# Kernel optimization log

Hardware: AMD Instinct MI355X
Metric: run time of the kernel (lower is better)

## Reference

```python
import jax, jax.numpy as jnp
import numpy as np


def _layernorm(x, g, b, eps=1e-6):
    mu = jnp.mean(x, -1, keepdims=True)
    var = jnp.var(x, -1, keepdims=True)
    return (x - mu) * jax.lax.rsqrt(var + eps) * g + b


def _rope_interleave(x, cos, sin):
    # de-interleave pairs (x0,x1),(x2,x3),... -> [evens | odds]  (matches
    # torch view(..., d//2, 2).transpose(-1,-2).reshape(..., d))
    x = jnp.concatenate([x[..., 0::2], x[..., 1::2]], axis=-1)
    d = x.shape[-1]
    x1, x2 = x[..., : d // 2], x[..., d // 2 :]
    rot = jnp.concatenate([-x2, x1], axis=-1)
    return x * cos + rot * sin


def setup_inputs() -> dict:
    key = jax.random.key(0)
    k = jax.random.split(key, 6)
    T, H, D, R, HID, QLR, K = 2048, 32, 128, 64, 4096, 1536, 256
    hidden_states = jax.random.normal(k[0], (1, T, HID), jnp.float32)
    q_latent = jax.random.normal(k[1], (1, T, QLR), jnp.float32)
    wq_b = jax.random.normal(k[2], (QLR, H * D), jnp.float32) * 0.02
    wk = jax.random.normal(k[3], (HID, D), jnp.float32) * 0.02
    w_proj = jax.random.normal(k[4], (HID, H), jnp.float32) * 0.02
    k_gamma = jnp.ones((D,), jnp.float32)
    k_beta = jnp.zeros((D,), jnp.float32)
    # real rotary cos/sin tables for the 64-dim rope slice
    pos = jnp.arange(T, dtype=jnp.float32)
    inv_freq = 1.0 / (10000.0 ** (jnp.arange(0, R, 2, dtype=jnp.float32) / R))
    freqs = jnp.outer(pos, inv_freq)
    emb = jnp.concatenate([freqs, freqs], axis=-1)  # [T, R]
    cos, sin = jnp.cos(emb), jnp.sin(emb)
    ks = jnp.zeros((T,), jnp.int32)
    ke = jnp.arange(1, T + 1, dtype=jnp.int32)  # causal: keys [0, t]
    return dict(hidden_states=hidden_states, q_latent=q_latent, ks=ks, ke=ke,
                cos=cos, sin=sin, wq_b=wq_b, wk=wk, k_gamma=k_gamma,
                k_beta=k_beta, w_proj=w_proj, index_topk=K)


def reference(hidden_states, q_latent, ks, ke, cos, sin, wq_b, wk,
              k_gamma, k_beta, w_proj, index_topk):
    T = hidden_states.shape[1]
    H = w_proj.shape[1]
    D = wk.shape[1]
    R = cos.shape[-1]
    weight_scale = (D ** -0.5) * (H ** -0.5)

    q = (q_latent[0] @ wq_b).reshape(T, H, D)              # [T,H,D]
    k = _layernorm(hidden_states[0] @ wk, k_gamma, k_beta)  # [T,D]
    w = hidden_states[0] @ w_proj                           # [T,H]

    q_pe = _rope_interleave(q[..., :R], cos[:, None, :], sin[:, None, :])
    k_pe = _rope_interleave(k[..., :R], cos, sin)
    q = jnp.concatenate([q_pe, q[..., R:]], axis=-1)
    k = jnp.concatenate([k_pe, k[..., R:]], axis=-1)

    # lightning-indexer score: I[t,s] = sum_h w[t,h] * relu(q[t,h] . k[s])
    scores = jnp.einsum('thd,sd->ths', q, k)                # [T,H,S]
    scores = jnp.einsum('ths,th->ts', jax.nn.relu(scores), w) * weight_scale

    j = jnp.arange(T)
    mask = (j[None, :] >= ks[:, None]) & (j[None, :] < ke[:, None])
    scores = jnp.where(mask, scores, -1e30)
    values, idx = jax.lax.top_k(scores, index_topk)
    return idx.reshape(1, T, 1, index_topk), values
```

## Files before the change

kernel.cpp:

```cpp
#include <hip/hip_runtime.h>
#include <cstdint>

typedef unsigned short u16;
typedef unsigned int   u32;
typedef unsigned long long u64;

typedef short bf16x8 __attribute__((ext_vector_type(8)));
typedef float f32x4  __attribute__((ext_vector_type(4)));
typedef u16   u16x8  __attribute__((ext_vector_type(8)));

__device__ __forceinline__ u16 f2b(float f){
  u32 u = __float_as_uint(f);
  u += 0x7FFFu + ((u >> 16) & 1u);
  return (u16)(u >> 16);
}
__device__ __forceinline__ float b2f(u16 h){ return __uint_as_float(((u32)h) << 16); }
__device__ __forceinline__ u32 fkey(float f){
  u32 u = __float_as_uint(f);
  return u ^ ((u & 0x80000000u) ? 0xFFFFFFFFu : 0x80000000u);
}
__device__ __forceinline__ float unkey(u32 k){
  u32 u = (k & 0x80000000u) ? (k ^ 0x80000000u) : ~k;
  return __uint_as_float(u);
}
__device__ __forceinline__ void gload16(const void* g, void* l){
  __builtin_amdgcn_global_load_lds(
      reinterpret_cast<const __attribute__((address_space(1))) char*>(reinterpret_cast<uintptr_t>(g)),
      reinterpret_cast<__attribute__((address_space(3))) char*>(reinterpret_cast<uintptr_t>(l)),
      16, 0, 0);
}

__global__ __launch_bounds__(256) void k_cvt(const float* __restrict__ in, u16* __restrict__ out, int n8){
  int i = blockIdx.x * 256 + threadIdx.x;
  if (i >= n8) return;
  const float4* p = (const float4*)in + (size_t)i * 2;
  float4 a = p[0], b = p[1];
  u16x8 v;
  v[0]=f2b(a.x); v[1]=f2b(a.y); v[2]=f2b(a.z); v[3]=f2b(a.w);
  v[4]=f2b(b.x); v[5]=f2b(b.y); v[6]=f2b(b.z); v[7]=f2b(b.w);
  *((u16x8*)out + i) = v;
}

__global__ __launch_bounds__(256) void k_tcvt(const float* __restrict__ in, u16* __restrict__ out, int R, int C){
  __shared__ float tile[32][33];
  int c0 = blockIdx.x * 32, r0 = blockIdx.y * 32;
  int tx = threadIdx.x & 31, ty = threadIdx.x >> 5;
  for (int i = 0; i < 4; i++){
    int r = ty * 4 + i;
    tile[r][tx] = in[(size_t)(r0 + r) * C + c0 + tx];
  }
  __syncthreads();
  for (int i = 0; i < 4; i++){
    int c = ty * 4 + i;
    out[(size_t)(c0 + c) * R + r0 + tx] = f2b(tile[tx][c]);
  }
}

__global__ __launch_bounds__(256) void k_wct(const float* __restrict__ wk, const float* __restrict__ wp, u16* __restrict__ out){
  __shared__ float tile[32][33];
  int c0 = blockIdx.x * 32, i0 = blockIdx.y * 32;
  int tx = threadIdx.x & 31, ty = threadIdx.x >> 5;
  for (int j = 0; j < 4; j++){
    int i = i0 + ty * 4 + j;
    int c = c0 + tx;
    float v = 0.f;
    if (c < 128) v = wk[(size_t)i * 128 + c];
    else if (c < 160) v = wp[(size_t)i * 32 + (c - 128)];
    tile[ty * 4 + j][tx] = v;
  }
  __syncthreads();
  for (int j = 0; j < 4; j++){
    int c = c0 + ty * 4 + j;
    out[(size_t)c * 4096 + i0 + tx] = f2b(tile[tx][ty * 4 + j]);
  }
}

__global__ __launch_bounds__(256) void k_gemm_kw(const float* __restrict__ A, const u16* __restrict__ B, float* __restrict__ Cp){
  const int Kd = 4096, NC = 192;
  __shared__ float As[128 * 64];
  __shared__ u16 Bs[64 * 64];
  int lin = blockIdx.x;
  int xcd = lin & 7, idx = lin >> 3;
  int nb = idx % 3, pz = idx / 3;
  int p = xcd + 8 * pz;
  int m0 = (p & 15) * 128;
  int kt0 = (p >> 4) * 512;
  int n0 = nb * 64;
  float* C = Cp + (size_t)(p >> 4) * 2048 * NC;
  int tid = threadIdx.x, lane = tid & 63, wid = tid >> 6;
  int wm = wid * 32;
  f32x4 acc[2][4] = {};
  for (int kt = kt0; kt < kt0 + 512; kt += 64){
    for (int c = tid; c < 2048; c += 256){
      int row = c >> 4, off = (c & 15) * 4;
      gload16(A + (size_t)(m0 + row) * Kd + kt + off, (float*)As + (size_t)c * 4);
    }
    for (int c = tid; c < 512; c += 256){
      int row = c >> 3, off = (c & 7) * 8;
      gload16(B + (size_t)(n0 + row) * Kd + kt + off, (u16*)Bs + (size_t)c * 8);
    }
    __syncthreads();
    for (int kk = 0; kk < 2; kk++){
      bf16x8 af[2], bfr[4];
      for (int i = 0; i < 2; i++){
        const float* src = &As[(wm + i * 16 + (lane & 15)) * 64 + kk * 32 + (lane >> 4) * 8];
        f32x4 lo = *(const f32x4*)&src[0];
        f32x4 hi = *(const f32x4*)&src[4];
        bf16x8 t;
        t[0]=(short)f2b(lo[0]); t[1]=(short)f2b(lo[1]); t[2]=(short)f2b(lo[2]); t[3]=(short)f2b(lo[3]);
        t[4]=(short)f2b(hi[0]); t[5]=(short)f2b(hi[1]); t[6]=(short)f2b(hi[2]); t[7]=(short)f2b(hi[3]);
        af[i] = t;
      }
      for (int j = 0; j < 4; j++)
        bfr[j] = *(const bf16x8*)&Bs[(j * 16 + (lane & 15)) * 64 + kk * 32 + (lane >> 4) * 8];
      for (int i = 0; i < 2; i++)
        for (int j = 0; j < 4; j++)
          acc[i][j] = __builtin_amdgcn_mfma_f32_16x16x32_bf16(af[i], bfr[j], acc[i][j], 0, 0, 0);
    }
    __syncthreads();
  }
  for (int i = 0; i < 2; i++)
    for (int j = 0; j < 4; j++){
      int row = m0 + wm + i * 16 + ((lane >> 4) * 4);
      int col = n0 + j * 16 + (lane & 15);
      for (int r = 0; r < 4; r++)
        C[(size_t)(row + r) * NC + col] = acc[i][j][r];
    }
}

__global__ __launch_bounds__(256) void k_lnrope(const float* __restrict__ kwp, const float* __restrict__ gamma,
                                                const float* __restrict__ beta, const float* __restrict__ cosp,
                                                const float* __restrict__ sinp, u16* __restrict__ krot,
                                                float* __restrict__ wfin){
  const size_t ZS = (size_t)2048 * 192;
  int row = blockIdx.x * 4 + (threadIdx.x >> 6);
  int lane = threadIdx.x & 63;
  const float* x = kwp + (size_t)row * 192;
  float2 v = {0.f, 0.f};
  for (int z = 0; z < 8; z++){
    float2 p = *(const float2*)&x[z * ZS + lane * 2];
    v.x += p.x; v.y += p.y;
  }
  float s = v.x + v.y, ss = v.x * v.x + v.y * v.y;
  for (int o = 32; o; o >>= 1){ s += __shfl_xor(s, o); ss += __shfl_xor(ss, o); }
  float mu = s * (1.f / 128.f);
  float var = ss * (1.f / 128.f) - mu * mu;
  float rs = rsqrtf(var + 1e-6f);
  float y0 = (v.x - mu) * rs * gamma[lane * 2]     + beta[lane * 2];
  float y1 = (v.y - mu) * rs * gamma[lane * 2 + 1] + beta[lane * 2 + 1];
  u16* out = krot + (size_t)row * 128;
  if (lane < 32){
    float c = cosp[(size_t)row * 64 + lane], sn = sinp[(size_t)row * 64 + lane];
    out[lane]      = f2b(y0 * c - y1 * sn);
    out[lane + 32] = f2b(y1 * c + y0 * sn);
    float wsum = 0.f;
    for (int z = 0; z < 8; z++) wsum += x[z * ZS + 128 + lane];
    wfin[(size_t)row * 32 + lane] = wsum;
  } else {
    out[lane * 2]     = f2b(y0);
    out[lane * 2 + 1] = f2b(y1);
  }
}

__global__ __launch_bounds__(256) void k_gemm_q(const u16* __restrict__ A, const u16* __restrict__ B,
                                                const float* __restrict__ cosp, const float* __restrict__ sinp,
                                                u16* __restrict__ C){
  const int N = 4096, Kd = 1536;
  __shared__ u16 As[128 * 64];
  __shared__ u16 Bs[128 * 64];
  int linb = blockIdx.x;
  int xcd = linb & 7, loc = linb >> 3;
  int n0 = (xcd * 4 + (loc >> 4)) * 128;
  int m0 = (loc & 15) * 128;
  int tid = threadIdx.x, lane = tid & 63, wid = tid >> 6;
  int wm = (wid >> 1) * 64, wn = (wid & 1) * 64;
  f32x4 acc[4][4] = {};
  for (int kt = 0; kt < Kd; kt += 64){
    for (int c = tid; c < 1024; c += 256){
      int row = c >> 3, off = (c & 7) * 8;
      gload16(A + (size_t)(m0 + row) * Kd + kt + off, (u16*)As + (size_t)c * 8);
      gload16(B + (size_t)(n0 + row) * Kd + kt + off, (u16*)Bs + (size_t)c * 8);
    }
    __syncthreads();
    for (int kk = 0; kk < 2; kk++){
      bf16x8 af[4], bfr[4];
      for (int i = 0; i < 4; i++){
        af[i]  = *(const bf16x8*)&As[(wm + i * 16 + (lane & 15)) * 64 + kk * 32 + (lane >> 4) * 8];
        bfr[i] = *(const bf16x8*)&Bs[(wn + i * 16 + (lane & 15)) * 64 + kk * 32 + (lane >> 4) * 8];
      }
      for (int i = 0; i < 4; i++)
        for (int j = 0; j < 4; j++)
          acc[i][j] = __builtin_amdgcn_mfma_f32_16x16x32_bf16(af[i], bfr[j], acc[i][j], 0, 0, 0);
    }
    __syncthreads();
  }
  if (wn == 0){
    int l = lane & 15;
    int base = lane & 48;
    int sl = base + ((2 * l) & 15);
    for (int i = 0; i < 4; i++){
      int rowb = m0 + wm + i * 16 + ((lane >> 4) * 4);
      f32x4 ne[4];
      for (int j = 0; j < 4; j++){
        int jj = j & 1;
        for (int r = 0; r < 4; r++){
          float eA = __shfl(acc[i][2 * jj][r],     sl);
          float eB = __shfl(acc[i][2 * jj + 1][r], sl);
          float oA = __shfl(acc[i][2 * jj][r],     sl + 1);
          float oB = __shfl(acc[i][2 * jj + 1][r], sl + 1);
          float e = (l >= 8) ? eB : eA;
          float o = (l >= 8) ? oB : oA;
          int row = rowb + r;
          int d = j * 16 + l;
          float c = cosp[(size_t)row * 64 + d];
          float s = sinp[(size_t)row * 64 + d];
          ne[j][r] = (j < 2) ? (e * c - o * s) : (o * c + e * s);
        }
      }
      for (int j = 0; j < 4; j++) acc[i][j] = ne[j];
    }
  }
  for (int i = 0; i < 4; i++)
    for (int j = 0; j < 4; j++){
      int row = m0 + wm + i * 16 + ((lane >> 4) * 4);
      int col = n0 + wn + j * 16 + (lane & 15);
      for (int r = 0; r < 4; r++)
        C[(size_t)(row + r) * N + col] = f2b(acc[i][j][r]);
    }
}

__global__ __launch_bounds__(256, 4) void k_scores(const u16* __restrict__ q, const u16* __restrict__ krot,
                                                   const float* __restrict__ wfin, const int* __restrict__ ke,
                                                   float* __restrict__ S0, float* __restrict__ S1){
  __shared__ u16 Bs[128 * 128];
  __shared__ float Ws[16][32];
  int bid = blockIdx.x;
  int xcd = bid & 7, loc = bid >> 3;
  int hgrp = loc & 1, rest = loc >> 1;
  int sb = rest & 15, j0 = rest >> 4;
  int tb = j0 * 8 + xcd;
  int t0 = tb * 32, s0 = sb * 128;
  int tid = threadIdx.x, lane = tid & 63, wid = tid >> 6;
  int wr = wid >> 1, wc = wid & 1;

  int kev = ke[t0 + (lane & 31)];
  int kemax = kev;
  for (int o = 16; o; o >>= 1) kemax = max(kemax, __shfl_xor(kemax, o));
  if (s0 >= kemax) return;

  for (int c = tid; c < 2048; c += 256)
    gload16(krot + (size_t)(s0 + (c >> 4)) * 128 + (c & 15) * 8, (u16*)Bs + (size_t)c * 8);
  for (int i = tid; i < 512; i += 256){
    int h = i >> 5, r = i & 31;
    Ws[h][r] = wfin[(size_t)(t0 + r) * 32 + hgrp * 16 + h];
  }
  __syncthreads();

  bf16x8 bfr[4][4];
  for (int j = 0; j < 4; j++)
    for (int kc = 0; kc < 4; kc++)
      bfr[j][kc] = *(const bf16x8*)&Bs[(wc * 64 + j * 16 + (lane & 15)) * 128 + kc * 32 + (lane >> 4) * 8];

  f32x4 acc[4] = {};
  const u16* qbase = q + ((size_t)t0 + wr * 16 + (lane & 15)) * 4096 + (size_t)hgrp * 16 * 128 + (lane >> 4) * 8;
  int rbase = wr * 16 + ((lane >> 4) * 4);
  for (int h = 0; h < 16; h++){
    bf16x8 af[4];
    for (int kc = 0; kc < 4; kc++)
      af[kc] = *(const bf16x8*)&qbase[h * 128 + kc * 32];
    f32x4 ah[4] = {};
    for (int kc = 0; kc < 4; kc++)
      for (int j = 0; j < 4; j++)
        ah[j] = __builtin_amdgcn_mfma_f32_16x16x32_bf16(af[kc], bfr[j][kc], ah[j], 0, 0, 0);
    for (int r = 0; r < 4; r++){
      float wv = Ws[h][rbase + r];
      for (int j = 0; j < 4; j++)
        acc[j][r] += fmaxf(ah[j][r], 0.f) * wv;
    }
  }
  float* Sp = hgrp ? S1 : S0;
  for (int j = 0; j < 4; j++){
    int col = s0 + wc * 64 + j * 16 + (lane & 15);
    for (int r = 0; r < 4; r++)
      Sp[(size_t)(t0 + rbase + r) * 2048 + col] = acc[j][r];
  }
}

__global__ __launch_bounds__(256) void k_topk(const float* __restrict__ S0, const float* __restrict__ S1,
                                              const int* __restrict__ ktp, const int* __restrict__ ksv,
                                              const int* __restrict__ ke, float* __restrict__ out){
  int t = blockIdx.x;
  int T = gridDim.x;
  const float* r0 = S0 + (size_t)t * 2048;
  const float* r1 = S1 + (size_t)t * 2048;
  __shared__ u32 keys[2048];
  __shared__ u32 hist[256];
  __shared__ u32 ssum[256];
  __shared__ u32 sb, srem;
  __shared__ u32 wtot[8];
  __shared__ int selIdx[256];
  __shared__ u32 baseGt, baseTie;
  __shared__ u64 skey[256];
  int tid = threadIdx.x;
  int K = ktp[0]; if (K > 256) K = 256;
  int ket = ke[t]; if (ket < 0) ket = 0; if (ket > 2048) ket = 2048;
  int kst = ksv[t]; if (kst < 0) kst = 0;
  int limit = (ket + 255) & ~255;
  if (limit < 256) limit = 256;
  if (limit > 2048) limit = 2048;
  const u32 kneg = fkey(-1e30f);
  const float scale = 0.015625f;
  for (int i4 = tid; i4 < (limit >> 2); i4 += 256){
    int base = i4 * 4;
    float4 a = ((const float4*)r0)[i4];
    float4 b = ((const float4*)r1)[i4];
    float v0 = (a.x + b.x) * scale, v1 = (a.y + b.y) * scale;
    float v2 = (a.z + b.z) * scale, v3 = (a.w + b.w) * scale;
    keys[base + 0] = (base + 0 >= kst && base + 0 < ket) ? fkey(v0) : kneg;
    keys[base + 1] = (base + 1 >= kst && base + 1 < ket) ? fkey(v1) : kneg;
    keys[base + 2] = (base + 2 >= kst && base + 2 < ket) ? fkey(v2) : kneg;
    keys[base + 3] = (base + 3 >= kst && base + 3 < ket) ? fkey(v3) : kneg;
  }
  __syncthreads();
  if (limit > K){
    u32 prefix = 0, pmask = 0, rem = (u32)K;
    for (int p = 3; p >= 0; p--){
      int sh = p * 8;
      hist[tid] = 0;
      __syncthreads();
      for (int i = tid; i < limit; i += 256){
        u32 u = keys[i];
        if ((u & pmask) == prefix) atomicAdd(&hist[(u >> sh) & 255], 1u);
      }
      __syncthreads();
      ssum[tid] = hist[tid];
      __syncthreads();
      for (int off = 1; off < 256; off <<= 1){
        u32 add = (tid + off < 256) ? ssum[tid + off] : 0u;
        __syncthreads();
        ssum[tid] += add;
        __syncthreads();
      }
      u32 mine = ssum[tid];
      u32 above = (tid == 255) ? 0u : ssum[tid + 1];
      if (mine >= rem && above < rem){ sb = (u32)tid; srem = rem - above; }
      __syncthreads();
      prefix |= (sb << sh);
      pmask |= (255u << sh);
      rem = srem;
      __syncthreads();
    }
    u32 thr = prefix;
    int G = K - (int)rem;
    if (tid == 0){ baseGt = 0; baseTie = 0; }
    __syncthreads();
    int nch = limit >> 8;
    for (int ch = 0; ch < nch; ch++){
      int i = ch * 256 + tid;
      u32 u = keys[i];
      bool gt = (u > thr), tie = (u == thr);
      u64 bg = __ballot(gt), bt = __ballot(tie);
      int lane = tid & 63, w = tid >> 6;
      if (lane == 0){ wtot[w] = (u32)__popcll(bg); wtot[4 + w] = (u32)__popcll(bt); }
      __syncthreads();
      u32 og = baseGt, ot = baseTie;
      for (int ww = 0; ww < w; ww++){ og += wtot[ww]; ot += wtot[4 + ww]; }
      og += (u32)__popcll(bg & ((1ull << lane) - 1ull));
      ot += (u32)__popcll(bt & ((1ull << lane) - 1ull));
      if (gt) selIdx[og] = i;
      else if (tie && ot < rem) selIdx[G + ot] = i;
      __syncthreads();
      if (tid == 0){
        for (int ww = 0; ww < 4; ww++){ baseGt += wtot[ww]; baseTie += wtot[4 + ww]; }
      }
      __syncthreads();
    }
    if (tid < K){
      int si = selIdx[tid];
      u32 u = keys[si];
      skey[tid] = ((u64)(~u) << 32) | (u32)si;
    } else {
      skey[tid] = ~0ull;
    }
  } else {
    if (tid < K) skey[tid] = ((u64)(~keys[tid]) << 32) | (u32)tid;
    else skey[tid] = ~0ull;
  }
  __syncthreads();
  for (int size = 2; size <= 256; size <<= 1){
    for (int stride = size >> 1; stride > 0; stride >>= 1){
      int p = tid ^ stride;
      if (p > tid){
        bool up = ((tid & size) == 0);
        u64 a = skey[tid], b = skey[p];
        if ((a > b) == up){ skey[tid] = b; skey[p] = a; }
      }
      __syncthreads();
    }
  }
  if (tid < K){
    u64 sk = skey[tid];
    int idx = (int)(u32)(sk & 0xFFFFFFFFu);
    float val = unkey(~(u32)(sk >> 32));
    out[(size_t)t * K + tid] = (float)idx;
    out[(size_t)T * K + (size_t)t * K + tid] = val;
  }
}

extern "C" void kernel_launch(void* const* d_in, const int* in_sizes, int n_in,
                              void* d_out, int out_size, void* d_ws, size_t ws_size,
                              hipStream_t stream){
  const float* hs   = (const float*)d_in[0];
  const float* ql   = (const float*)d_in[1];
  const int*   ks   = (const int*)  d_in[2];
  const int*   ke   = (const int*)  d_in[3];
  const float* cosp = (const float*)d_in[4];
  const float* sinp = (const float*)d_in[5];
  const float* wqb  = (const float*)d_in[6];
  const float* wk   = (const float*)d_in[7];
  const float* kg   = (const float*)d_in[8];
  const float* kb   = (const float*)d_in[9];
  const float* wp   = (const float*)d_in[10];
  const int*   ktp  = (const int*)  d_in[11];

  char* w = (char*)d_ws;
  u16* qlb = (u16*)w;  w += (size_t)2048 * 1536 * 2;
  u16* wqT = (u16*)w;  w += (size_t)4096 * 1536 * 2;
  u16* wct = (u16*)w;  w += (size_t)192 * 4096 * 2;
  u16* qb  = (u16*)w;  w += (size_t)2048 * 4096 * 2;
  float* kwp = (float*)w; w += (size_t)8 * 2048 * 192 * 4;
  float* wfin = (float*)w; w += (size_t)2048 * 32 * 4;
  u16* krt = (u16*)w;  w += (size_t)2048 * 128 * 2;
  float* S0 = (float*)w; w += (size_t)2048 * 2048 * 4;
  float* S1 = (float*)d_ws;

  hipLaunchKernelGGL(k_cvt, dim3(1536), dim3(256), 0, stream, ql, qlb, 393216);
  hipLaunchKernelGGL(k_tcvt, dim3(128, 48), dim3(256), 0, stream, wqb, wqT, 1536, 4096);
  hipLaunchKernelGGL(k_wct, dim3(6, 128), dim3(256), 0, stream, wk, wp, wct);
  hipLaunchKernelGGL(k_gemm_kw, dim3(384), dim3(256), 0, stream, hs, wct, kwp);
  hipLaunchKernelGGL(k_lnrope, dim3(512), dim3(256), 0, stream, kwp, kg, kb, cosp, sinp, krt, wfin);
  hipLaunchKernelGGL(k_gemm_q, dim3(512), dim3(256), 0, stream, qlb, wqT, cosp, sinp, qb);
  hipLaunchKernelGGL(k_scores, dim3(2048), dim3(256), 0, stream, qb, krt, wfin, ke, S0, S1);
  hipLaunchKernelGGL(k_topk, dim3(2048), dim3(256), 0, stream, S0, S1, ktp, ks, ke, (float*)d_out);
}
```

Measured before the change: 163.0 us.

## Drop head-group split in scores kernel; tile over key blocks instead

The scores kernel previously split the 32 heads into two groups and wrote two partial score matrices that top-k summed. Each block now covers all 32 heads for a 64-key tile, which halves the score write and read traffic and removes the partial-sum add in top-k. Key tiles are narrower, giving finer causal early exit, but each block does twice as many head iterations with half the MFMA columns and reuses each q load over fewer keys.

```diff
diff --git a/kernel.cpp b/kernel.cpp
--- a/kernel.cpp
+++ b/kernel.cpp
@@ -231,15 +231,14 @@
 
 __global__ __launch_bounds__(256, 4) void k_scores(const u16* __restrict__ q, const u16* __restrict__ krot,
                                                    const float* __restrict__ wfin, const int* __restrict__ ke,
-                                                   float* __restrict__ S0, float* __restrict__ S1){
-  __shared__ u16 Bs[128 * 128];
-  __shared__ float Ws[16][32];
+                                                   float* __restrict__ S){
+  __shared__ u16 Bs[64 * 128];
+  __shared__ float Ws[32][32];
   int bid = blockIdx.x;
   int xcd = bid & 7, loc = bid >> 3;
-  int hgrp = loc & 1, rest = loc >> 1;
-  int sb = rest & 15, j0 = rest >> 4;
+  int sb = loc & 31, j0 = loc >> 5;
   int tb = j0 * 8 + xcd;
-  int t0 = tb * 32, s0 = sb * 128;
+  int t0 = tb * 32, s0 = sb * 64;
   int tid = threadIdx.x, lane = tid & 63, wid = tid >> 6;
   int wr = wid >> 1, wc = wid & 1;
 
@@ -248,51 +247,49 @@
   for (int o = 16; o; o >>= 1) kemax = max(kemax, __shfl_xor(kemax, o));
   if (s0 >= kemax) return;
 
-  for (int c = tid; c < 2048; c += 256)
+  for (int c = tid; c < 1024; c += 256)
     gload16(krot + (size_t)(s0 + (c >> 4)) * 128 + (c & 15) * 8, (u16*)Bs + (size_t)c * 8);
-  for (int i = tid; i < 512; i += 256){
+  for (int i = tid; i < 1024; i += 256){
     int h = i >> 5, r = i & 31;
-    Ws[h][r] = wfin[(size_t)(t0 + r) * 32 + hgrp * 16 + h];
+    Ws[h][r] = wfin[(size_t)(t0 + r) * 32 + h];
   }
   __syncthreads();
 
-  bf16x8 bfr[4][4];
-  for (int j = 0; j < 4; j++)
+  bf16x8 bfr[2][4];
+  for (int j = 0; j < 2; j++)
     for (int kc = 0; kc < 4; kc++)
-      bfr[j][kc] = *(const bf16x8*)&Bs[(wc * 64 + j * 16 + (lane & 15)) * 128 + kc * 32 + (lane >> 4) * 8];
-
-  f32x4 acc[4] = {};
-  const u16* qbase = q + ((size_t)t0 + wr * 16 + (lane & 15)) * 4096 + (size_t)hgrp * 16 * 128 + (lane >> 4) * 8;
+      bfr[j][kc] = *(const bf16x8*)&Bs[(wc * 32 + j * 16 + (lane & 15)) * 128 + kc * 32 + (lane >> 4) * 8];
+
+  f32x4 acc[2] = {};
+  const u16* qbase = q + ((size_t)t0 + wr * 16 + (lane & 15)) * 4096 + (lane >> 4) * 8;
   int rbase = wr * 16 + ((lane >> 4) * 4);
-  for (int h = 0; h < 16; h++){
+  for (int h = 0; h < 32; h++){
     bf16x8 af[4];
     for (int kc = 0; kc < 4; kc++)
       af[kc] = *(const bf16x8*)&qbase[h * 128 + kc * 32];
-    f32x4 ah[4] = {};
+    f32x4 ah[2] = {};
     for (int kc = 0; kc < 4; kc++)
-      for (int j = 0; j < 4; j++)
+      for (int j = 0; j < 2; j++)
         ah[j] = __builtin_amdgcn_mfma_f32_16x16x32_bf16(af[kc], bfr[j][kc], ah[j], 0, 0, 0);
     for (int r = 0; r < 4; r++){
       float wv = Ws[h][rbase + r];
-      for (int j = 0; j < 4; j++)
+      for (int j = 0; j < 2; j++)
         acc[j][r] += fmaxf(ah[j][r], 0.f) * wv;
     }
   }
-  float* Sp = hgrp ? S1 : S0;
-  for (int j = 0; j < 4; j++){
-    int col = s0 + wc * 64 + j * 16 + (lane & 15);
+  for (int j = 0; j < 2; j++){
+    int col = s0 + wc * 32 + j * 16 + (lane & 15);
     for (int r = 0; r < 4; r++)
-      Sp[(size_t)(t0 + rbase + r) * 2048 + col] = acc[j][r];
-  }
-}
-
-__global__ __launch_bounds__(256) void k_topk(const float* __restrict__ S0, const float* __restrict__ S1,
-                                              const int* __restrict__ ktp, const int* __restrict__ ksv,
-                                              const int* __restrict__ ke, float* __restrict__ out){
+      S[(size_t)(t0 + rbase + r) * 2048 + col] = acc[j][r];
+  }
+}
+
+__global__ __launch_bounds__(256) void k_topk(const float* __restrict__ S, const int* __restrict__ ktp,
+                                              const int* __restrict__ ksv, const int* __restrict__ ke,
+                                              float* __restrict__ out){
   int t = blockIdx.x;
   int T = gridDim.x;
-  const float* r0 = S0 + (size_t)t * 2048;
-  const float* r1 = S1 + (size_t)t * 2048;
+  const float* row = S + (size_t)t * 2048;
   __shared__ u32 keys[2048];
   __shared__ u32 hist[256];
   __shared__ u32 ssum[256];
@@ -312,14 +309,11 @@
   const float scale = 0.015625f;
   for (int i4 = tid; i4 < (limit >> 2); i4 += 256){
     int base = i4 * 4;
-    float4 a = ((const float4*)r0)[i4];
-    float4 b = ((const float4*)r1)[i4];
-    float v0 = (a.x + b.x) * scale, v1 = (a.y + b.y) * scale;
-    float v2 = (a.z + b.z) * scale, v3 = (a.w + b.w) * scale;
-    keys[base + 0] = (base + 0 >= kst && base + 0 < ket) ? fkey(v0) : kneg;
-    keys[base + 1] = (base + 1 >= kst && base + 1 < ket) ? fkey(v1) : kneg;
-    keys[base + 2] = (base + 2 >= kst && base + 2 < ket) ? fkey(v2) : kneg;
-    keys[base + 3] = (base + 3 >= kst && base + 3 < ket) ? fkey(v3) : kneg;
+    float4 a = ((const float4*)row)[i4];
+    keys[base + 0] = (base + 0 >= kst && base + 0 < ket) ? fkey(a.x * scale) : kneg;
+    keys[base + 1] = (base + 1 >= kst && base + 1 < ket) ? fkey(a.y * scale) : kneg;
+    keys[base + 2] = (base + 2 >= kst && base + 2 < ket) ? fkey(a.z * scale) : kneg;
+    keys[base + 3] = (base + 3 >= kst && base + 3 < ket) ? fkey(a.w * scale) : kneg;
   }
   __syncthreads();
   if (limit > K){
@@ -431,8 +425,7 @@
   float* kwp = (float*)w; w += (size_t)8 * 2048 * 192 * 4;
   float* wfin = (float*)w; w += (size_t)2048 * 32 * 4;
   u16* krt = (u16*)w;  w += (size_t)2048 * 128 * 2;
-  float* S0 = (float*)w; w += (size_t)2048 * 2048 * 4;
-  float* S1 = (float*)d_ws;
+  float* S  = (float*)w; w += (size_t)2048 * 2048 * 4;
 
   hipLaunchKernelGGL(k_cvt, dim3(1536), dim3(256), 0, stream, ql, qlb, 393216);
   hipLaunchKernelGGL(k_tcvt, dim3(128, 48), dim3(256), 0, stream, wqb, wqT, 1536, 4096);
@@ -440,6 +433,6 @@
   hipLaunchKernelGGL(k_gemm_kw, dim3(384), dim3(256), 0, stream, hs, wct, kwp);
   hipLaunchKernelGGL(k_lnrope, dim3(512), dim3(256), 0, stream, kwp, kg, kb, cosp, sinp, krt, wfin);
   hipLaunchKernelGGL(k_gemm_q, dim3(512), dim3(256), 0, stream, qlb, wqT, cosp, sinp, qb);
-  hipLaunchKernelGGL(k_scores, dim3(2048), dim3(256), 0, stream, qb, krt, wfin, ke, S0, S1);
-  hipLaunchKernelGGL(k_topk, dim3(2048), dim3(256), 0, stream, S0, S1, ktp, ks, ke, (float*)d_out);
-}
+  hipLaunchKernelGGL(k_scores, dim3(2048), dim3(256), 0, stream, qb, krt, wfin, ke, S);
+  hipLaunchKernelGGL(k_topk, dim3(2048), dim3(256), 0, stream, S, ktp, ks, ke, (float*)d_out);
+}
```

New measurement: 217.5 us. 1.33x slower.
